# Kernel optimization log

Hardware: AMD Instinct MI355X
Metric: run time of the kernel (lower is better)

## Reference

```python
import jax, jax.numpy as jnp
import numpy as np

N_HEADS = 16
D_K = 64
MAX_LEN = 5000


def setup_inputs() -> dict:
    key = jax.random.key(0)
    ks = jax.random.split(key, 6)
    B, L, D = 4, 1024, 1024
    s = 1.0 / np.sqrt(D).astype(np.float32)
    return {
        "x": jax.random.normal(ks[0], (B, L, D), jnp.float32),
        "W_q": jax.random.normal(ks[1], (D, D), jnp.float32) * s,
        "b_q": jnp.zeros((D,), jnp.float32),
        "W_k": jax.random.normal(ks[2], (D, D), jnp.float32) * s,
        "b_k": jnp.zeros((D,), jnp.float32),
        "W_v": jax.random.normal(ks[3], (D, D), jnp.float32) * s,
        "b_v": jnp.zeros((D,), jnp.float32),
        "W_o": jax.random.normal(ks[4], (D, D), jnp.float32) * s,
        "b_o": jnp.zeros((D,), jnp.float32),
        "Er": jax.random.normal(ks[5], (MAX_LEN, D_K), jnp.float32) * 0.02,
    }


def reference(x, W_q, b_q, W_k, b_k, W_v, b_v, W_o, b_o, Er):
    B, L, D = x.shape
    H = N_HEADS
    dk = D // H
    # torch nn.Linear: y = x @ W.T + b
    Q = (x @ W_q.T + b_q).reshape(B, L, H, dk).transpose(0, 2, 1, 3)  # (B,H,L,dk)
    K = (x @ W_k.T + b_k).reshape(B, L, H, dk).transpose(0, 2, 1, 3)
    V = (x @ W_v.T + b_v).reshape(B, L, H, dk).transpose(0, 2, 1, 3)
    AC = jnp.einsum('bhid,bhjd->bhij', Q, K)  # (B,H,L,L)
    rel_pos = jnp.arange(L - 1, -L, -1) + (MAX_LEN - 1)  # (2L-1,)
    # mode='clip' matches intended math: clamped rows fall in the part that
    # the relative shift slices away.
    Er_embed = jnp.take(Er, rel_pos, axis=0, mode='clip')  # (2L-1, dk)
    BD = jnp.einsum('bhid,rd->bhir', Q, Er_embed)  # (B,H,L,2L-1)
    # _relative_shift: view is a no-op (shape already (B,H,L,2L-1)), then slice
    BD = BD[..., L - 1:]  # (B,H,L,L)
    scores = (AC + BD) / np.sqrt(dk).astype(np.float32)
    attn = jax.nn.softmax(scores, axis=-1)
    out = jnp.einsum('bhij,bhjd->bhid', attn, V)
    out = out.transpose(0, 2, 1, 3).reshape(B, L, D)
    return out @ W_o.T + b_o
```

## Files before the change

### kernel.cpp

```cpp
#include <hip/hip_runtime.h>
#include <cstdint>
#include <cstddef>


typedef __attribute__((ext_vector_type(8))) short short8;
typedef __attribute__((ext_vector_type(4))) float f32x4;

#define MFMA_BF16(a, b, c) __builtin_amdgcn_mfma_f32_16x16x32_bf16((a), (b), (c), 0, 0, 0)

constexpr int kB = 4, kL = 1024, kD = 1024, kH = 16;
constexpr int kBL = kB * kL;
constexpr float kScale = 0.125f * 1.44269504088896340736f;

static __device__ __forceinline__ unsigned short f32_to_bf16(float f) {
  union { float f; uint32_t u; } c; c.f = f;
  uint32_t u = c.u + 0x7fffu + ((c.u >> 16) & 1u);
  return (unsigned short)(u >> 16);
}

static __device__ __forceinline__ void gload_lds16(const void* g, void* l) {
  __builtin_amdgcn_global_load_lds(
      (const __attribute__((address_space(1))) void*)g,
      (__attribute__((address_space(3))) void*)l, 16, 0, 0);
}

__global__ __launch_bounds__(256)
void cast_all(const float* __restrict__ x,  const float* __restrict__ Wq,
              const float* __restrict__ Wk, const float* __restrict__ Wv,
              const float* __restrict__ Wo,
              unsigned short* __restrict__ xb, unsigned short* __restrict__ Wcat,
              unsigned short* __restrict__ Wob) {
  int i = blockIdx.x * blockDim.x + threadIdx.x;
  const float* src;
  ushort4* dst;
  int off;
  if (i < 1048576) {
    src = x; dst = reinterpret_cast<ushort4*>(xb); off = i;
  } else {
    int j = i - 1048576;
    int seg = j >> 18;
    off = j & 262143;
    if (seg == 0)      { src = Wq; dst = reinterpret_cast<ushort4*>(Wcat); }
    else if (seg == 1) { src = Wk; dst = reinterpret_cast<ushort4*>(Wcat) + 262144; }
    else if (seg == 2) { src = Wv; dst = reinterpret_cast<ushort4*>(Wcat) + 524288; }
    else               { src = Wo; dst = reinterpret_cast<ushort4*>(Wob); }
  }
  float4 v = reinterpret_cast<const float4*>(src)[off];
  ushort4 o;
  o.x = f32_to_bf16(v.x); o.y = f32_to_bf16(v.y);
  o.z = f32_to_bf16(v.z); o.w = f32_to_bf16(v.w);
  dst[off] = o;
}

__global__ __launch_bounds__(256)
void gemm_qkv(const unsigned short* __restrict__ A,
              const unsigned short* __restrict__ Bm,
              const float* __restrict__ bq, const float* __restrict__ bk,
              const float* __restrict__ bv,
              const float* __restrict__ Er,
              unsigned short* __restrict__ Qh, unsigned short* __restrict__ Kh,
              unsigned short* __restrict__ Vth) {
  __shared__ __align__(16) char smem[32768];
  unsigned short* As = (unsigned short*)smem;
  unsigned short* Bs = (unsigned short*)(smem + 16384);
  const int tid  = threadIdx.x;
  const int lane = tid & 63, wave = tid >> 6;
  const int quad = lane >> 4, l15 = lane & 15;
  const int m0 = blockIdx.y * 128, n0 = blockIdx.x * 128;
  const int wm = (wave >> 1) * 64, wn = (wave & 1) * 64;
  const int K = 1024;

  const f32x4 vzero = {0.f, 0.f, 0.f, 0.f};
  f32x4 acc[4][4];
#pragma unroll
  for (int i = 0; i < 4; ++i)
#pragma unroll
    for (int j = 0; j < 4; ++j) acc[i][j] = vzero;

  for (int k0 = 0; k0 < K; k0 += 64) {
    __syncthreads();
#pragma unroll
    for (int j = 0; j < 4; ++j) {
      int u = j * 256 + tid;
      int half = u >> 9, row = (u >> 2) & 127, c = (u & 3) * 8 + half * 32;
      gload_lds16(A  + (size_t)(m0 + row) * K + k0 + c, (char*)As + (size_t)u * 16);
      gload_lds16(Bm + (size_t)(n0 + row) * K + k0 + c, (char*)Bs + (size_t)u * 16);
    }
    __syncthreads();

#pragma unroll
    for (int ks = 0; ks < 2; ++ks) {
      short8 af[4], bfv[4];
#pragma unroll
      for (int mt = 0; mt < 4; ++mt)
        af[mt] = *(const short8*)&As[ks * 4096 + (wm + mt * 16 + l15) * 32 + quad * 8];
#pragma unroll
      for (int nt = 0; nt < 4; ++nt)
        bfv[nt] = *(const short8*)&Bs[ks * 4096 + (wn + nt * 16 + l15) * 32 + quad * 8];
#pragma unroll
      for (int mt = 0; mt < 4; ++mt)
#pragma unroll
        for (int nt = 0; nt < 4; ++nt)
          acc[mt][nt] = MFMA_BF16(af[mt], bfv[nt], acc[mt][nt]);
    }
  }

  const int wsel = n0 >> 10;
  const int b   = (m0 + wm) >> 10;
  const int i0l = (m0 + wm) & 1023;
  const int nl0 = (n0 & 1023) + wn;
  const int h   = nl0 >> 6;
  const size_t bh = (size_t)(b * 16 + h);

  if (wsel == 0) {
#pragma unroll
    for (int mt = 0; mt < 4; ++mt)
#pragma unroll
      for (int nt = 0; nt < 4; ++nt)
#pragma unroll
        for (int r = 0; r < 4; ++r) {
          const int i = i0l + mt * 16 + quad * 4 + r;
          const int n = nl0 + nt * 16 + l15;
          float v = (acc[mt][nt][r] + bq[n]) * kScale;
          Qh[(bh * 1024 + i) * 64 + (n & 63)] = f32_to_bf16(v);
        }
  } else if (wsel == 1) {
#pragma unroll
    for (int mt = 0; mt < 4; ++mt)
#pragma unroll
      for (int nt = 0; nt < 4; ++nt)
#pragma unroll
        for (int r = 0; r < 4; ++r) {
          const int i = i0l + mt * 16 + quad * 4 + r;
          const int n = nl0 + nt * 16 + l15;
          const int d = n & 63;
          float v = acc[mt][nt][r] + bk[n] + Er[(size_t)(4999 - i) * 64 + d];
          Kh[(bh * 1024 + i) * 64 + d] = f32_to_bf16(v);
        }
  } else {
    __syncthreads();
    unsigned short* W = (unsigned short*)smem + (size_t)wave * 4096;
#pragma unroll
    for (int mt = 0; mt < 4; ++mt)
#pragma unroll
      for (int nt = 0; nt < 4; ++nt) {
        ushort4 pk;
        const int n = nl0 + nt * 16 + l15;
        pk.x = f32_to_bf16(acc[mt][nt][0] + bv[n]);
        pk.y = f32_to_bf16(acc[mt][nt][1] + bv[n]);
        pk.z = f32_to_bf16(acc[mt][nt][2] + bv[n]);
        pk.w = f32_to_bf16(acc[mt][nt][3] + bv[n]);
        *(ushort4*)&W[(size_t)(nt * 16 + l15) * 64 + mt * 16 + quad * 4] = pk;
      }
#pragma unroll
    for (int p = 0; p < 8; ++p) {
      const int u = p * 64 + lane;
      const int d = u >> 3, ch = (u & 7) * 8;
      short8 vv = *(const short8*)&W[(size_t)d * 64 + ch];
      *(short8*)&Vth[(bh * 64 + d) * 1024 + i0l + ch] = vv;
    }
  }
}

__global__ __launch_bounds__(256)
void gemm_out(const unsigned short* __restrict__ A,
              const unsigned short* __restrict__ Bm,
              const float* __restrict__ bias,
              float* __restrict__ outf) {
  __shared__ unsigned short As[2][128 * 32];
  __shared__ unsigned short Bs[2][64 * 32];
  const int tid  = threadIdx.x;
  const int lane = tid & 63, wave = tid >> 6;
  const int quad = lane >> 4, l15 = lane & 15;
  const int m0 = blockIdx.y * 128, n0 = blockIdx.x * 64;
  const int K = 1024;

  const f32x4 vzero = {0.f, 0.f, 0.f, 0.f};
  f32x4 acc[2][4];
#pragma unroll
  for (int i = 0; i < 2; ++i)
#pragma unroll
    for (int j = 0; j < 4; ++j) acc[i][j] = vzero;

  for (int k0 = 0; k0 < K; k0 += 64) {
    __syncthreads();
#pragma unroll
    for (int j = 0; j < 4; ++j) {
      int u = j * 256 + tid;
      int half = u >> 9, row = (u >> 2) & 127, c = (u & 3) * 8 + half * 32;
      gload_lds16(A + (size_t)(m0 + row) * K + k0 + c, (char*)&As[0][0] + (size_t)u * 16);
    }
#pragma unroll
    for (int j = 0; j < 2; ++j) {
      int u = j * 256 + tid;
      int half = u >> 8, row = (u >> 2) & 63, c = (u & 3) * 8 + half * 32;
      gload_lds16(Bm + (size_t)(n0 + row) * K + k0 + c, (char*)&Bs[0][0] + (size_t)u * 16);
    }
    __syncthreads();

#pragma unroll
    for (int ks = 0; ks < 2; ++ks) {
      short8 af[2], bfv[4];
#pragma unroll
      for (int mt = 0; mt < 2; ++mt)
        af[mt] = *(const short8*)&As[ks][(wave * 32 + mt * 16 + l15) * 32 + quad * 8];
#pragma unroll
      for (int nt = 0; nt < 4; ++nt)
        bfv[nt] = *(const short8*)&Bs[ks][(nt * 16 + l15) * 32 + quad * 8];
#pragma unroll
      for (int mt = 0; mt < 2; ++mt)
#pragma unroll
        for (int nt = 0; nt < 4; ++nt)
          acc[mt][nt] = MFMA_BF16(af[mt], bfv[nt], acc[mt][nt]);
    }
  }

#pragma unroll
  for (int mt = 0; mt < 2; ++mt)
#pragma unroll
    for (int nt = 0; nt < 4; ++nt)
#pragma unroll
      for (int r = 0; r < 4; ++r) {
        const int gm = m0 + wave * 32 + mt * 16 + quad * 4 + r;
        const int gn = n0 + nt * 16 + l15;
        outf[(size_t)gm * 1024 + gn] = acc[mt][nt][r] + bias[gn];
      }
}

__global__ __launch_bounds__(256)
void attn_kernel(const unsigned short* __restrict__ Q,
                 const unsigned short* __restrict__ Kp,
                 const unsigned short* __restrict__ Vt,
                 unsigned short* __restrict__ Ao) {
  __shared__ unsigned short Ks[2][2][64 * 32];
  __shared__ unsigned short Vs[2][2][64 * 32];
  __shared__ unsigned short Plds[4][32 * 72];
  const int tid  = threadIdx.x;
  const int lane = tid & 63, wave = tid >> 6;
  const int quad = lane >> 4, l15 = lane & 15;
  const int bh = blockIdx.x;
  const int qb = blockIdx.y;
  const size_t base  = (size_t)bh * (kL * 64);
  const size_t vbase = (size_t)bh * (64 * kL);
  const int i0 = qb * 128 + wave * 32;

  short8 qf[2][2];
#pragma unroll
  for (int mt = 0; mt < 2; ++mt)
#pragma unroll
    for (int ks = 0; ks < 2; ++ks)
      qf[mt][ks] = *(const short8*)
          &Q[base + (size_t)(i0 + mt * 16 + l15) * 64 + ks * 32 + quad * 8];

  auto stage = [&](int buf, int kb) {
#pragma unroll
    for (int j = 0; j < 2; ++j) {
      int u = j * 256 + tid;
      int half = u >> 8, row = (u >> 2) & 63, c = (u & 3) * 8;
      gload_lds16(Kp + base + (size_t)(kb * 64 + row) * 64 + half * 32 + c,
                  (char*)&Ks[buf][0][0] + (size_t)u * 16);
      gload_lds16(Vt + vbase + (size_t)row * kL + kb * 64 + half * 32 + c,
                  (char*)&Vs[buf][0][0] + (size_t)u * 16);
    }
  };

  const f32x4 vzero = {0.f, 0.f, 0.f, 0.f};
  f32x4 of[2][4];
#pragma unroll
  for (int mt = 0; mt < 2; ++mt)
#pragma unroll
    for (int dt = 0; dt < 4; ++dt) of[mt][dt] = vzero;
  float lsum[2][4] = {{0.f, 0.f, 0.f, 0.f}, {0.f, 0.f, 0.f, 0.f}};

  unsigned short* Pw = Plds[wave];

  stage(0, 0);
  __syncthreads();

  for (int kb = 0; kb < 16; ++kb) {
    const int cur = kb & 1, nxt = cur ^ 1;
    if (kb < 15) stage(nxt, kb + 1);

    short8 kf[4][2];
#pragma unroll
    for (int nt = 0; nt < 4; ++nt)
#pragma unroll
      for (int ks = 0; ks < 2; ++ks)
        kf[nt][ks] = *(const short8*)&Ks[cur][ks][(nt * 16 + l15) * 32 + quad * 8];
    f32x4 sf[2][4];
#pragma unroll
    for (int mt = 0; mt < 2; ++mt)
#pragma unroll
      for (int nt = 0; nt < 4; ++nt) {
        sf[mt][nt] = MFMA_BF16(qf[mt][0], kf[nt][0], vzero);
        sf[mt][nt] = MFMA_BF16(qf[mt][1], kf[nt][1], sf[mt][nt]);
      }

#pragma unroll
    for (int mt = 0; mt < 2; ++mt)
#pragma unroll
      for (int nt = 0; nt < 4; ++nt)
#pragma unroll
        for (int r = 0; r < 4; ++r) {
          float p = __builtin_amdgcn_exp2f(sf[mt][nt][r]);
          lsum[mt][r] += p;
          union { float f; uint32_t u; } c; c.f = p;
          Pw[(mt * 16 + quad * 4 + r) * 72 + nt * 16 + l15] =
              (unsigned short)((c.u + 0x8000u) >> 16);
        }
    short8 pf[2][2];
#pragma unroll
    for (int mt = 0; mt < 2; ++mt)
#pragma unroll
      for (int ks = 0; ks < 2; ++ks)
        pf[mt][ks] = *(const short8*)&Pw[(mt * 16 + l15) * 72 + ks * 32 + quad * 8];

    short8 vf[4][2];
#pragma unroll
    for (int dt = 0; dt < 4; ++dt)
#pragma unroll
      for (int ks = 0; ks < 2; ++ks)
        vf[dt][ks] = *(const short8*)&Vs[cur][ks][(dt * 16 + l15) * 32 + quad * 8];
#pragma unroll
    for (int mt = 0; mt < 2; ++mt)
#pragma unroll
      for (int dt = 0; dt < 4; ++dt) {
        of[mt][dt] = MFMA_BF16(pf[mt][0], vf[dt][0], of[mt][dt]);
        of[mt][dt] = MFMA_BF16(pf[mt][1], vf[dt][1], of[mt][dt]);
      }

    __syncthreads();
  }

#pragma unroll
  for (int mask = 1; mask < 16; mask <<= 1)
#pragma unroll
    for (int mt = 0; mt < 2; ++mt)
#pragma unroll
      for (int r = 0; r < 4; ++r)
        lsum[mt][r] += __shfl_xor(lsum[mt][r], mask);
  float rl[2][4];
#pragma unroll
  for (int mt = 0; mt < 2; ++mt)
#pragma unroll
    for (int r = 0; r < 4; ++r) rl[mt][r] = __builtin_amdgcn_rcpf(lsum[mt][r]);

  const int b = bh >> 4, h = bh & 15;
#pragma unroll
  for (int mt = 0; mt < 2; ++mt)
#pragma unroll
    for (int dt = 0; dt < 4; ++dt)
#pragma unroll
      for (int r = 0; r < 4; ++r) {
        const int ig = i0 + mt * 16 + quad * 4 + r;
        float v = of[mt][dt][r] * rl[mt][r];
        Ao[((size_t)(b * 1024 + ig)) * 1024 + h * 64 + dt * 16 + l15] = f32_to_bf16(v);
      }
}

extern "C" void kernel_launch(void* const* d_in, const int* in_sizes, int n_in,
                              void* d_out, int out_size, void* d_ws, size_t ws_size,
                              hipStream_t stream) {
  const float* x   = (const float*)d_in[0];
  const float* W_q = (const float*)d_in[1];
  const float* b_q = (const float*)d_in[2];
  const float* W_k = (const float*)d_in[3];
  const float* b_k = (const float*)d_in[4];
  const float* W_v = (const float*)d_in[5];
  const float* b_v = (const float*)d_in[6];
  const float* W_o = (const float*)d_in[7];
  const float* b_o = (const float*)d_in[8];
  const float* Er  = (const float*)d_in[9];
  float* out = (float*)d_out;

  char* ws = (char*)d_ws;
  unsigned short* xb   = (unsigned short*)(ws + (size_t)0);
  unsigned short* Wcat = (unsigned short*)(ws + ((size_t)8  << 20));
  unsigned short* Wob  = (unsigned short*)(ws + ((size_t)14 << 20));
  unsigned short* Qh   = (unsigned short*)(ws + ((size_t)16 << 20));
  unsigned short* Kh   = (unsigned short*)(ws + ((size_t)24 << 20));
  unsigned short* Vth  = (unsigned short*)(ws + ((size_t)32 << 20));
  unsigned short* Aoh  = (unsigned short*)(ws + ((size_t)40 << 20));

  cast_all<<<8192, 256, 0, stream>>>(x, W_q, W_k, W_v, W_o, xb, Wcat, Wob);

  gemm_qkv<<<dim3(24, 32), 256, 0, stream>>>(
      xb, Wcat, b_q, b_k, b_v, Er, Qh, Kh, Vth);

  attn_kernel<<<dim3(kB * kH, kL / 128), 256, 0, stream>>>(Qh, Kh, Vth, Aoh);

  gemm_out<<<dim3(16, 32), 256, 0, stream>>>(Aoh, Wob, b_o, out);
}
```

Before: 188.1 us.

## Rewrite QKV GEMM with 256x256 tiles, double-buffered LDS pipeline and XCD-aware mapping

```diff
diff --git a/kernel.cpp b/kernel.cpp
--- a/kernel.cpp
+++ b/kernel.cpp
@@ -52,7 +52,7 @@
   dst[off] = o;
 }
 
-__global__ __launch_bounds__(256)
+__global__ __launch_bounds__(512, 2)
 void gemm_qkv(const unsigned short* __restrict__ A,
               const unsigned short* __restrict__ Bm,
               const float* __restrict__ bq, const float* __restrict__ bk,
@@ -60,103 +60,162 @@
               const float* __restrict__ Er,
               unsigned short* __restrict__ Qh, unsigned short* __restrict__ Kh,
               unsigned short* __restrict__ Vth) {
-  __shared__ __align__(16) char smem[32768];
-  unsigned short* As = (unsigned short*)smem;
-  unsigned short* Bs = (unsigned short*)(smem + 16384);
+  __shared__ __align__(16) char smem[131072];
   const int tid  = threadIdx.x;
   const int lane = tid & 63, wave = tid >> 6;
-  const int quad = lane >> 4, l15 = lane & 15;
-  const int m0 = blockIdx.y * 128, n0 = blockIdx.x * 128;
-  const int wm = (wave >> 1) * 64, wn = (wave & 1) * 64;
-  const int K = 1024;
+  const int quad = lane >> 4, l15 = lane & 15, lhalf = l15 >> 1;
+  const int wr = wave >> 2, wc = wave & 3;
+
+  const int bid = blockIdx.x;
+  const int xcd = bid & 7, idx = bid >> 3;
+  const int mt_ = idx / 6, nt_ = idx - mt_ * 6;
+  const int m0 = ((xcd >> 1) * 4 + mt_) * 256;
+  const int n0 = ((xcd & 1) * 6 + nt_) * 256;
+
+  const int lane_off = (l15 & 1) * 64 + ((quad * 16) ^ ((lhalf & 3) << 4));
+  const int aoff = lhalf * 128 + lane_off + wr * 8192;
+  const int boff = lhalf * 128 + lane_off + wc * 4096;
+
+  int srow[2], scol[2];
+#pragma unroll
+  for (int j = 0; j < 2; ++j) {
+    int poff = (j * 512 + tid) * 16;
+    int L = poff ^ (((poff >> 7) & 3) << 4);
+    srow[j] = ((L >> 7) << 1) | ((L >> 6) & 1);
+    scol[j] = (L & 63) >> 1;
+  }
+
+  auto stageAB = [&](int X, int kh, int tt) {
+    const unsigned short* src = X ? Bm : A;
+    const int rbase = X ? n0 : m0;
+    char* dst = smem + ((tt & 1) * 65536 + X * 32768 + kh * 16384) + tid * 16;
+    const int kc = tt * 64 + kh * 32;
+#pragma unroll
+    for (int j = 0; j < 2; ++j)
+      gload_lds16(src + (size_t)(rbase + srow[j]) * 1024 + kc + scol[j],
+                  dst + j * 8192);
+  };
 
   const f32x4 vzero = {0.f, 0.f, 0.f, 0.f};
-  f32x4 acc[4][4];
-#pragma unroll
-  for (int i = 0; i < 4; ++i)
+  f32x4 acc[8][4];
+#pragma unroll
+  for (int i = 0; i < 8; ++i)
 #pragma unroll
     for (int j = 0; j < 4; ++j) acc[i][j] = vzero;
 
-  for (int k0 = 0; k0 < K; k0 += 64) {
-    __syncthreads();
-#pragma unroll
-    for (int j = 0; j < 4; ++j) {
-      int u = j * 256 + tid;
-      int half = u >> 9, row = (u >> 2) & 127, c = (u & 3) * 8 + half * 32;
-      gload_lds16(A  + (size_t)(m0 + row) * K + k0 + c, (char*)As + (size_t)u * 16);
-      gload_lds16(Bm + (size_t)(n0 + row) * K + k0 + c, (char*)Bs + (size_t)u * 16);
-    }
-    __syncthreads();
-
-#pragma unroll
-    for (int ks = 0; ks < 2; ++ks) {
-      short8 af[4], bfv[4];
-#pragma unroll
-      for (int mt = 0; mt < 4; ++mt)
-        af[mt] = *(const short8*)&As[ks * 4096 + (wm + mt * 16 + l15) * 32 + quad * 8];
-#pragma unroll
-      for (int nt = 0; nt < 4; ++nt)
-        bfv[nt] = *(const short8*)&Bs[ks * 4096 + (wn + nt * 16 + l15) * 32 + quad * 8];
-#pragma unroll
-      for (int mt = 0; mt < 4; ++mt)
-#pragma unroll
-        for (int nt = 0; nt < 4; ++nt)
-          acc[mt][nt] = MFMA_BF16(af[mt], bfv[nt], acc[mt][nt]);
-    }
-  }
+  stageAB(0, 0, 0); stageAB(1, 0, 0); stageAB(0, 1, 0); stageAB(1, 1, 0);
+  stageAB(0, 0, 1); stageAB(1, 0, 1);
+  asm volatile("s_waitcnt vmcnt(4)" ::: "memory");
+  __builtin_amdgcn_s_barrier();
+
+#define LDA(KH, MB) do {                                                      \
+    _Pragma("unroll")                                                         \
+    for (int f_ = 0; f_ < 4; ++f_)                                            \
+      af[f_] = *(const short8*)(RA + (KH) * 16384 + aoff + ((MB) + f_) * 1024); \
+  } while (0)
+#define LDB(KH) do {                                                          \
+    _Pragma("unroll")                                                         \
+    for (int n_ = 0; n_ < 4; ++n_)                                            \
+      bf[n_] = *(const short8*)(RB + (KH) * 16384 + boff + n_ * 1024);        \
+  } while (0)
+#define BARA() do {                                                           \
+    __builtin_amdgcn_s_barrier();                                             \
+    asm volatile("s_waitcnt lgkmcnt(0)" ::: "memory");                        \
+    __builtin_amdgcn_sched_barrier(0);                                        \
+  } while (0)
+#define MFMA_QUAD(MB) do {                                                    \
+    __builtin_amdgcn_s_setprio(1);                                            \
+    _Pragma("unroll")                                                         \
+    for (int mq_ = 0; mq_ < 4; ++mq_) {                                       \
+      _Pragma("unroll")                                                       \
+      for (int nq_ = 0; nq_ < 4; ++nq_)                                       \
+        acc[(MB) + mq_][nq_] =                                                \
+            MFMA_BF16(af[mq_], bf[nq_], acc[(MB) + mq_][nq_]);                \
+    }                                                                         \
+    __builtin_amdgcn_s_setprio(0);                                            \
+  } while (0)
+
+  for (int t = 0; t < 16; ++t) {
+    const char* RA = smem + (t & 1) * 65536;
+    const char* RB = RA + 32768;
+    short8 af[4], bf[4];
+    LDA(0, 0); LDB(0);
+    if (t + 1 < 16) stageAB(0, 1, t + 1);
+    BARA(); MFMA_QUAD(0);
+    __builtin_amdgcn_s_barrier();
+    LDA(0, 4);
+    if (t + 1 < 16) stageAB(1, 1, t + 1);
+    BARA(); MFMA_QUAD(4);
+    __builtin_amdgcn_s_barrier();
+    LDA(1, 0); LDB(1);
+    if (t + 2 < 16) stageAB(0, 0, t + 2);
+    BARA(); MFMA_QUAD(0);
+    __builtin_amdgcn_s_barrier();
+    LDA(1, 4);
+    if (t + 2 < 16) stageAB(1, 0, t + 2);
+    BARA(); MFMA_QUAD(4);
+    if (t < 14) asm volatile("s_waitcnt vmcnt(4)" ::: "memory");
+    else        asm volatile("s_waitcnt vmcnt(0)" ::: "memory");
+    __builtin_amdgcn_s_barrier();
+  }
+
+#undef LDA
+#undef LDB
+#undef BARA
+#undef MFMA_QUAD
 
   const int wsel = n0 >> 10;
-  const int b   = (m0 + wm) >> 10;
-  const int i0l = (m0 + wm) & 1023;
-  const int nl0 = (n0 & 1023) + wn;
-  const int h   = nl0 >> 6;
-  const size_t bh = (size_t)(b * 16 + h);
+  const int gmb  = m0 + wr * 128;
+  const int bb   = gmb >> 10, i0l = gmb & 1023;
+  const int nl0  = (n0 & 1023) + wc * 64;
+  const int hh   = nl0 >> 6;
+  const size_t bh = (size_t)(bb * 16 + hh);
 
   if (wsel == 0) {
 #pragma unroll
-    for (int mt = 0; mt < 4; ++mt)
-#pragma unroll
-      for (int nt = 0; nt < 4; ++nt)
+    for (int mf = 0; mf < 8; ++mf)
+#pragma unroll
+      for (int nf = 0; nf < 4; ++nf)
 #pragma unroll
         for (int r = 0; r < 4; ++r) {
-          const int i = i0l + mt * 16 + quad * 4 + r;
-          const int n = nl0 + nt * 16 + l15;
-          float v = (acc[mt][nt][r] + bq[n]) * kScale;
+          const int i = i0l + mf * 16 + quad * 4 + r;
+          const int n = nl0 + nf * 16 + l15;
+          float v = (acc[mf][nf][r] + bq[n]) * kScale;
           Qh[(bh * 1024 + i) * 64 + (n & 63)] = f32_to_bf16(v);
         }
   } else if (wsel == 1) {
 #pragma unroll
-    for (int mt = 0; mt < 4; ++mt)
-#pragma unroll
-      for (int nt = 0; nt < 4; ++nt)
+    for (int mf = 0; mf < 8; ++mf)
+#pragma unroll
+      for (int nf = 0; nf < 4; ++nf)
 #pragma unroll
         for (int r = 0; r < 4; ++r) {
-          const int i = i0l + mt * 16 + quad * 4 + r;
-          const int n = nl0 + nt * 16 + l15;
+          const int i = i0l + mf * 16 + quad * 4 + r;
+          const int n = nl0 + nf * 16 + l15;
           const int d = n & 63;
-          float v = acc[mt][nt][r] + bk[n] + Er[(size_t)(4999 - i) * 64 + d];
+          float v = acc[mf][nf][r] + bk[n] + Er[(size_t)(4999 - i) * 64 + d];
           Kh[(bh * 1024 + i) * 64 + d] = f32_to_bf16(v);
         }
   } else {
     __syncthreads();
-    unsigned short* W = (unsigned short*)smem + (size_t)wave * 4096;
-#pragma unroll
-    for (int mt = 0; mt < 4; ++mt)
-#pragma unroll
-      for (int nt = 0; nt < 4; ++nt) {
+    unsigned short* W = (unsigned short*)smem + (size_t)wave * 8192;
+#pragma unroll
+    for (int mf = 0; mf < 8; ++mf)
+#pragma unroll
+      for (int nf = 0; nf < 4; ++nf) {
         ushort4 pk;
-        const int n = nl0 + nt * 16 + l15;
-        pk.x = f32_to_bf16(acc[mt][nt][0] + bv[n]);
-        pk.y = f32_to_bf16(acc[mt][nt][1] + bv[n]);
-        pk.z = f32_to_bf16(acc[mt][nt][2] + bv[n]);
-        pk.w = f32_to_bf16(acc[mt][nt][3] + bv[n]);
-        *(ushort4*)&W[(size_t)(nt * 16 + l15) * 64 + mt * 16 + quad * 4] = pk;
+        const int n = nl0 + nf * 16 + l15;
+        pk.x = f32_to_bf16(acc[mf][nf][0] + bv[n]);
+        pk.y = f32_to_bf16(acc[mf][nf][1] + bv[n]);
+        pk.z = f32_to_bf16(acc[mf][nf][2] + bv[n]);
+        pk.w = f32_to_bf16(acc[mf][nf][3] + bv[n]);
+        *(ushort4*)&W[(size_t)(nf * 16 + l15) * 128 + mf * 16 + quad * 4] = pk;
       }
 #pragma unroll
-    for (int p = 0; p < 8; ++p) {
+    for (int p = 0; p < 16; ++p) {
       const int u = p * 64 + lane;
-      const int d = u >> 3, ch = (u & 7) * 8;
-      short8 vv = *(const short8*)&W[(size_t)d * 64 + ch];
+      const int d = u >> 4, ch = (u & 15) * 8;
+      short8 vv = *(const short8*)&W[(size_t)d * 128 + ch];
       *(short8*)&Vth[(bh * 64 + d) * 1024 + i0l + ch] = vv;
     }
   }
@@ -384,7 +443,7 @@
 
   cast_all<<<8192, 256, 0, stream>>>(x, W_q, W_k, W_v, W_o, xb, Wcat, Wob);
 
-  gemm_qkv<<<dim3(24, 32), 256, 0, stream>>>(
+  gemm_qkv<<<192, 512, 0, stream>>>(
       xb, Wcat, b_q, b_k, b_v, Er, Qh, Kh, Vth);
 
   attn_kernel<<<dim3(kB * kH, kL / 128), 256, 0, stream>>>(Qh, Kh, Vth, Aoh);
```

After: 175.6 us. 1.07x faster.
